# Performance work log

Hardware: AMD Instinct MI355X
Metric: run time of the kernel (lower is better)

Reference implementation:

```python
import jax, jax.numpy as jnp
import numpy as np

# Plane axes from generate_planes(); projection uses their inverses (permutation matrices).
_PLANES = np.array([[[1, 0, 0], [0, 1, 0], [0, 0, 1]],
                    [[1, 0, 0], [0, 0, 1], [0, 1, 0]],
                    [[0, 0, 1], [1, 0, 0], [0, 1, 0]]], dtype=np.float32)
_INV_PLANES = np.linalg.inv(_PLANES)  # [3,3,3]


def _grid_sample_2d(feat, grid):
    """Bilinear grid_sample, padding_mode='zeros', align_corners=False.
    feat: [C,H,W], grid: [M,2] with (x,y) in normalized coords. Returns [C,M]."""
    C, H, W = feat.shape
    x = ((grid[:, 0] + 1.0) * W - 1.0) * 0.5  # [M] pixel coords
    y = ((grid[:, 1] + 1.0) * H - 1.0) * 0.5
    x0 = jnp.floor(x)
    y0 = jnp.floor(y)
    wx = x - x0  # weight of right/bottom neighbor
    wy = y - y0
    x0i = x0.astype(jnp.int32)
    y0i = y0.astype(jnp.int32)
    x1i = x0i + 1
    y1i = y0i + 1

    def corner(xi, yi):
        valid = (xi >= 0) & (xi < W) & (yi >= 0) & (yi < H)
        xc = jnp.clip(xi, 0, W - 1)
        yc = jnp.clip(yi, 0, H - 1)
        v = feat[:, yc, xc]  # [C, M] gather
        return v * valid.astype(feat.dtype)

    v00 = corner(x0i, y0i)
    v10 = corner(x1i, y0i)
    v01 = corner(x0i, y1i)
    v11 = corner(x1i, y1i)
    out = (v00 * (1.0 - wx) * (1.0 - wy)
           + v10 * wx * (1.0 - wy)
           + v01 * (1.0 - wx) * wy
           + v11 * wx * wy)
    return out  # [C, M]


def setup_inputs() -> dict:
    key = jax.random.key(0)
    k1, k2, k3 = jax.random.split(key, 3)
    N, P, C, H, W, M = 4, 3, 32, 256, 256, 500000
    planes = jax.random.normal(k1, (N, P, C, H, W), dtype=jnp.float32)
    sample_coordinates = jax.random.uniform(k2, (N, M, 3), dtype=jnp.float32,
                                            minval=-1.0, maxval=1.0)
    sample_directions = jax.random.normal(k3, (N, M, 3), dtype=jnp.float32)
    return {"planes": planes, "sample_coordinates": sample_coordinates,
            "sample_directions": sample_directions}


def reference(planes, sample_coordinates, sample_directions):
    # ImportanceRenderer.run_model: project -> grid_sample per plane -> mean over planes.
    N, n_planes, C, H, W = planes.shape
    M = sample_coordinates.shape[1]
    inv = jnp.asarray(_INV_PLANES, dtype=sample_coordinates.dtype)  # [P,3,3]
    # torch.bmm(coords, inv_planes): [N,P,M,3] @ [P,3,3] -> take first 2 dims
    proj = jnp.einsum('nmi,pij->npmj', sample_coordinates, inv)[..., :2]  # [N,P,M,2]
    feats = planes.reshape(N * n_planes, C, H, W)
    grids = proj.reshape(N * n_planes, M, 2)
    sampled = jax.vmap(_grid_sample_2d)(feats, grids)  # [N*P, C, M]
    sampled = sampled.reshape(N, n_planes, C, M).transpose(0, 1, 3, 2)  # [N,P,M,C]
    return sampled.mean(axis=1)  # [N, M, C]
```

## Files before the change

### kernel.cpp

```cpp
#include <hip/hip_runtime.h>
#include <hip/hip_fp16.h>


constexpr int Cc = 32, Hh = 256, Ww = 256, Pp = 3, Nn = 4;
constexpr int HWPIX = Hh * Ww;
constexpr int NCO   = 4096;
constexpr int CAP   = 256;

typedef float f32x4 __attribute__((ext_vector_type(4)));

__device__ inline unsigned spread3(unsigned x) {
    x &= 0x3FFu;
    x = (x | (x << 16)) & 0x030000FFu;
    x = (x | (x << 8))  & 0x0300F00Fu;
    x = (x | (x << 4))  & 0x030C30C3u;
    x = (x | (x << 2))  & 0x09249249u;
    return x;
}
__device__ inline unsigned coarse_key(float cx, float cy, float cz) {
    const int a = min(max((int)((cx + 1.0f) * 8.0f), 0), 15);
    const int b = min(max((int)((cy + 1.0f) * 8.0f), 0), 15);
    const int c = min(max((int)((cz + 1.0f) * 8.0f), 0), 15);
    return spread3((unsigned)a) | (spread3((unsigned)b) << 1) | (spread3((unsigned)c) << 2);
}

__global__ __launch_bounds__(256) void transpose_chw_hwc_h(
    const float* __restrict__ in, __half* __restrict__ out)
{
    __shared__ float lds[Cc * 257];
    const int slice = blockIdx.y;
    const int pix0  = blockIdx.x * 256;
    const int t     = threadIdx.x;

    const float* src = in + (size_t)slice * Cc * HWPIX + pix0 + t;
    #pragma unroll
    for (int c = 0; c < Cc; ++c)
        lds[c * 257 + t] = src[(size_t)c * HWPIX];
    __syncthreads();

    uint4* dst = reinterpret_cast<uint4*>(
        out + (size_t)slice * HWPIX * Cc + (size_t)pix0 * Cc);
    #pragma unroll
    for (int k = 0; k < 4; ++k) {
        const int idx = k * 256 + t;
        const int pix = idx >> 2;
        const int c0  = (idx & 3) * 8;
        unsigned r[4];
        #pragma unroll
        for (int j = 0; j < 4; ++j) {
            const __half h0 = __float2half(lds[(c0 + 2 * j + 0) * 257 + pix]);
            const __half h1 = __float2half(lds[(c0 + 2 * j + 1) * 257 + pix]);
            r[j] = (unsigned)__half_as_ushort(h0)
                 | ((unsigned)__half_as_ushort(h1) << 16);
        }
        dst[idx] = make_uint4(r[0], r[1], r[2], r[3]);
    }
}

__global__ __launch_bounds__(256) void zero_u32(unsigned* __restrict__ p, int n)
{
    const int i = blockIdx.x * 256 + threadIdx.x;
    if (i < n) p[i] = 0u;
}

__global__ __launch_bounds__(256) void bin_scatter(
    const float* __restrict__ coords, unsigned* __restrict__ count,
    unsigned* __restrict__ tailcnt, unsigned* __restrict__ bin,
    unsigned* __restrict__ tail, int M)
{
    const int m = blockIdx.x * 256 + threadIdx.x;
    const int n = blockIdx.y;
    if (m >= M) return;
    const float* cp = coords + ((size_t)n * M + m) * 3;
    const unsigned k = coarse_key(cp[0], cp[1], cp[2]);
    const unsigned r = atomicAdd(&count[n * NCO + k], 1u);
    if (r < CAP) {
        bin[(((size_t)n * NCO + k) << 8) + r] = (unsigned)m;
    } else {
        const unsigned t = atomicAdd(&tailcnt[n], 1u);
        tail[(size_t)n * M + t] = (unsigned)m;
    }
}

__global__ __launch_bounds__(1024) void cell_scan_base(
    const unsigned* __restrict__ count, unsigned* __restrict__ base)
{
    __shared__ unsigned lds[1024];
    const unsigned* h = count + (size_t)blockIdx.x * NCO;
    unsigned* o = base + (size_t)blockIdx.x * NCO;
    const int t = threadIdx.x;
    unsigned v[4];
    unsigned s = 0;
    #pragma unroll
    for (int i = 0; i < 4; ++i) { v[i] = min(h[t * 4 + i], (unsigned)CAP); s += v[i]; }
    lds[t] = s;
    __syncthreads();
    for (int d = 1; d < 1024; d <<= 1) {
        const unsigned add = (t >= d) ? lds[t - d] : 0u;
        __syncthreads();
        lds[t] += add;
        __syncthreads();
    }
    unsigned b = (t > 0) ? lds[t - 1] : 0u;
    #pragma unroll
    for (int i = 0; i < 4; ++i) { const unsigned tmp = v[i]; o[t * 4 + i] = b; b += tmp; }
}

__global__ __launch_bounds__(256) void compact_cells(
    const unsigned* __restrict__ count, const unsigned* __restrict__ base,
    const unsigned* __restrict__ bin, unsigned* __restrict__ dense, int M)
{
    const int n = blockIdx.y, cell = blockIdx.x, t = threadIdx.x;
    const unsigned c = min(count[n * NCO + cell], (unsigned)CAP);
    if ((unsigned)t < c)
        dense[(size_t)n * M + base[n * NCO + cell] + t] =
            bin[(((size_t)n * NCO + cell) << 8) + t];
}

__global__ __launch_bounds__(256) void tail_copy(
    const unsigned* __restrict__ tailcnt, const unsigned* __restrict__ tail,
    unsigned* __restrict__ dense, int M)
{
    const int n = blockIdx.x;
    const unsigned tc = tailcnt[n];
    for (unsigned t = threadIdx.x; t < tc; t += 256)
        dense[(size_t)n * M + (M - tc) + t] = tail[(size_t)n * M + t];
}

__global__ __launch_bounds__(256) void triplane_gather4h(
    const __half* __restrict__ tp, const unsigned* __restrict__ idx,
    const float* __restrict__ coords, float* __restrict__ out,
    int M, int gx, int nwg)
{
    int bid = blockIdx.x;
    {
        const int q = nwg >> 3, r = nwg & 7;
        const int xcd = bid & 7, i = bid >> 3;
        bid = (xcd < r ? xcd * (q + 1) : r * (q + 1) + (xcd - r) * q) + i;
    }
    const int n  = bid / gx;
    const int bx = bid - n * gx;
    const int gid  = bx * 256 + threadIdx.x;
    const int s    = gid >> 2;
    const int quad = gid & 3;
    if (s >= M) return;

    const int m = (int)idx[(size_t)n * M + s];
    const float* cp = coords + ((size_t)n * M + m) * 3;
    const float cx = cp[0], cy = cp[1], cz = cp[2];

    const uint4* addr[12];
    __half2 wh[12];

    #pragma unroll
    for (int p = 0; p < 3; ++p) {
        const float gxc = (p == 2) ? cz : cx;
        const float gyc = (p == 0) ? cy : ((p == 1) ? cz : cx);
        const float x = ((gxc + 1.0f) * 256.0f - 1.0f) * 0.5f;
        const float y = ((gyc + 1.0f) * 256.0f - 1.0f) * 0.5f;
        const float x0f = floorf(x), y0f = floorf(y);
        const float wx = x - x0f, wy = y - y0f;
        const int x0 = (int)x0f, y0 = (int)y0f;
        const int x1 = x0 + 1,   y1 = y0 + 1;
        const bool vx0 = (unsigned)x0 < 256u;
        const bool vx1 = (unsigned)x1 < 256u;
        const bool vy0 = (unsigned)y0 < 256u;
        const bool vy1 = (unsigned)y1 < 256u;
        const int cx0 = min(max(x0, 0), 255), cx1 = min(max(x1, 0), 255);
        const int cy0 = min(max(y0, 0), 255), cy1 = min(max(y1, 0), 255);

        const float w00 = ((vx0 && vy0) ? 1.f : 0.f) * (1.f - wx) * (1.f - wy);
        const float w10 = ((vx1 && vy0) ? 1.f : 0.f) * wx * (1.f - wy);
        const float w01 = ((vx0 && vy1) ? 1.f : 0.f) * (1.f - wx) * wy;
        const float w11 = ((vx1 && vy1) ? 1.f : 0.f) * wx * wy;
        wh[p * 4 + 0] = __float2half2_rn(w00);
        wh[p * 4 + 1] = __float2half2_rn(w10);
        wh[p * 4 + 2] = __float2half2_rn(w01);
        wh[p * 4 + 3] = __float2half2_rn(w11);

        const uint4* base = reinterpret_cast<const uint4*>(
            tp + (size_t)(n * 3 + p) * HWPIX * Cc);
        addr[p * 4 + 0] = base + (size_t)((cy0 << 8) + cx0) * 4 + quad;
        addr[p * 4 + 1] = base + (size_t)((cy0 << 8) + cx1) * 4 + quad;
        addr[p * 4 + 2] = base + (size_t)((cy1 << 8) + cx0) * 4 + quad;
        addr[p * 4 + 3] = base + (size_t)((cy1 << 8) + cx1) * 4 + quad;
    }

    uint4 rv[12];
    #pragma unroll
    for (int j = 0; j < 12; ++j) rv[j] = *addr[j];

    float accx[8];
    #pragma unroll
    for (int i = 0; i < 8; ++i) accx[i] = 0.f;

    #pragma unroll
    for (int p = 0; p < 3; ++p) {
        __half2 a0 = __float2half2_rn(0.f), a1 = a0, a2 = a0, a3 = a0;
        #pragma unroll
        for (int c = 0; c < 4; ++c) {
            const uint4 v = rv[p * 4 + c];
            const __half2 w = wh[p * 4 + c];
            a0 = __hfma2(*reinterpret_cast<const __half2*>(&v.x), w, a0);
            a1 = __hfma2(*reinterpret_cast<const __half2*>(&v.y), w, a1);
            a2 = __hfma2(*reinterpret_cast<const __half2*>(&v.z), w, a2);
            a3 = __hfma2(*reinterpret_cast<const __half2*>(&v.w), w, a3);
        }
        const float2 f0 = __half22float2(a0);
        const float2 f1 = __half22float2(a1);
        const float2 f2 = __half22float2(a2);
        const float2 f3 = __half22float2(a3);
        accx[0] += f0.x; accx[1] += f0.y;
        accx[2] += f1.x; accx[3] += f1.y;
        accx[4] += f2.x; accx[5] += f2.y;
        accx[6] += f3.x; accx[7] += f3.y;
    }

    constexpr float third = 1.0f / 3.0f;
    f32x4 o0, o1;
    o0.x = accx[0] * third; o0.y = accx[1] * third;
    o0.z = accx[2] * third; o0.w = accx[3] * third;
    o1.x = accx[4] * third; o1.y = accx[5] * third;
    o1.z = accx[6] * third; o1.w = accx[7] * third;

    f32x4* op = reinterpret_cast<f32x4*>(out + ((size_t)n * M + m) * Cc);
    __builtin_nontemporal_store(o0, op + quad * 2 + 0);
    __builtin_nontemporal_store(o1, op + quad * 2 + 1);
}

__global__ __launch_bounds__(256) void triplane_gather_hwc8h(
    const __half* __restrict__ tp, const float* __restrict__ coords,
    float* __restrict__ out, int M)
{
    const int gid   = blockIdx.x * 256 + threadIdx.x;
    const int m     = gid >> 3;
    const int chunk = gid & 7;
    const int n     = blockIdx.y;
    if (m >= M) return;

    const float* cp = coords + ((size_t)n * M + m) * 3;
    const float cx = cp[0], cy = cp[1], cz = cp[2];

    const uint2* addr[12];
    float w[12];

    #pragma unroll
    for (int p = 0; p < 3; ++p) {
        const float gxc = (p == 2) ? cz : cx;
        const float gyc = (p == 0) ? cy : ((p == 1) ? cz : cx);
        const float x = ((gxc + 1.0f) * 256.0f - 1.0f) * 0.5f;
        const float y = ((gyc + 1.0f) * 256.0f - 1.0f) * 0.5f;
        const float x0f = floorf(x), y0f = floorf(y);
        const float wx = x - x0f, wy = y - y0f;
        const int x0 = (int)x0f, y0 = (int)y0f;
        const int x1 = x0 + 1,   y1 = y0 + 1;
        const bool vx0 = (unsigned)x0 < 256u;
        const bool vx1 = (unsigned)x1 < 256u;
        const bool vy0 = (unsigned)y0 < 256u;
        const bool vy1 = (unsigned)y1 < 256u;
        const int cx0 = min(max(x0, 0), 255), cx1 = min(max(x1, 0), 255);
        const int cy0 = min(max(y0, 0), 255), cy1 = min(max(y1, 0), 255);

        w[p * 4 + 0] = ((vx0 && vy0) ? 1.f : 0.f) * (1.f - wx) * (1.f - wy);
        w[p * 4 + 1] = ((vx1 && vy0) ? 1.f : 0.f) * wx * (1.f - wy);
        w[p * 4 + 2] = ((vx0 && vy1) ? 1.f : 0.f) * (1.f - wx) * wy;
        w[p * 4 + 3] = ((vx1 && vy1) ? 1.f : 0.f) * wx * wy;

        const uint2* base = reinterpret_cast<const uint2*>(
            tp + (size_t)(n * 3 + p) * HWPIX * Cc);
        addr[p * 4 + 0] = base + (size_t)((cy0 << 8) + cx0) * 8 + chunk;
        addr[p * 4 + 1] = base + (size_t)((cy0 << 8) + cx1) * 8 + chunk;
        addr[p * 4 + 2] = base + (size_t)((cy1 << 8) + cx0) * 8 + chunk;
        addr[p * 4 + 3] = base + (size_t)((cy1 << 8) + cx1) * 8 + chunk;
    }

    uint2 rv[12];
    #pragma unroll
    for (int j = 0; j < 12; ++j) rv[j] = *addr[j];

    float4 acc = make_float4(0.f, 0.f, 0.f, 0.f);
    #pragma unroll
    for (int j = 0; j < 12; ++j) {
        const __half2 h0 = *reinterpret_cast<const __half2*>(&rv[j].x);
        const __half2 h1 = *reinterpret_cast<const __half2*>(&rv[j].y);
        const float2 f0 = __half22float2(h0);
        const float2 f1 = __half22float2(h1);
        acc.x += w[j] * f0.x;
        acc.y += w[j] * f0.y;
        acc.z += w[j] * f1.x;
        acc.w += w[j] * f1.y;
    }

    constexpr float third = 1.0f / 3.0f;
    acc.x *= third; acc.y *= third; acc.z *= third; acc.w *= third;

    float4* op = reinterpret_cast<float4*>(out + ((size_t)n * M + m) * Cc);
    op[chunk] = acc;
}

__global__ __launch_bounds__(256) void triplane_gather_chw(
    const float* __restrict__ planes, const float* __restrict__ coords,
    float* __restrict__ out, int M)
{
    const int m = blockIdx.x * 256 + threadIdx.x;
    const int n = blockIdx.y;
    if (m >= M) return;

    const float* cp = coords + ((size_t)n * M + m) * 3;
    const float cx = cp[0], cy = cp[1], cz = cp[2];

    int   off[3][4];
    float w[3][4];
    #pragma unroll
    for (int p = 0; p < 3; ++p) {
        const float gxc = (p == 2) ? cz : cx;
        const float gyc = (p == 0) ? cy : ((p == 1) ? cz : cx);
        const float x = ((gxc + 1.0f) * 256.0f - 1.0f) * 0.5f;
        const float y = ((gyc + 1.0f) * 256.0f - 1.0f) * 0.5f;
        const float x0f = floorf(x), y0f = floorf(y);
        const float wx = x - x0f, wy = y - y0f;
        const int x0 = (int)x0f, y0 = (int)y0f;
        const int x1 = x0 + 1,   y1 = y0 + 1;
        const bool vx0 = (unsigned)x0 < 256u, vx1 = (unsigned)x1 < 256u;
        const bool vy0 = (unsigned)y0 < 256u, vy1 = (unsigned)y1 < 256u;
        const int cx0 = min(max(x0, 0), 255), cx1 = min(max(x1, 0), 255);
        const int cy0 = min(max(y0, 0), 255), cy1 = min(max(y1, 0), 255);
        off[p][0] = (cy0 << 8) + cx0;  w[p][0] = ((vx0 && vy0) ? 1.f : 0.f) * (1.f - wx) * (1.f - wy);
        off[p][1] = (cy0 << 8) + cx1;  w[p][1] = ((vx1 && vy0) ? 1.f : 0.f) * wx * (1.f - wy);
        off[p][2] = (cy1 << 8) + cx0;  w[p][2] = ((vx0 && vy1) ? 1.f : 0.f) * (1.f - wx) * wy;
        off[p][3] = (cy1 << 8) + cx1;  w[p][3] = ((vx1 && vy1) ? 1.f : 0.f) * wx * wy;
    }

    float* op = out + ((size_t)n * M + m) * Cc;
    constexpr float third = 1.0f / 3.0f;
    for (int c = 0; c < Cc; ++c) {
        float a = 0.f;
        #pragma unroll
        for (int p = 0; p < 3; ++p) {
            const float* b = planes + ((size_t)(n * 3 + p) * Cc + c) * HWPIX;
            a += w[p][0] * b[off[p][0]] + w[p][1] * b[off[p][1]]
               + w[p][2] * b[off[p][2]] + w[p][3] * b[off[p][3]];
        }
        op[c] = a * third;
    }
}

extern "C" void kernel_launch(void* const* d_in, const int* in_sizes, int n_in,
                              void* d_out, int out_size, void* d_ws, size_t ws_size,
                              hipStream_t stream)
{
    const float* planes = (const float*)d_in[0];
    const float* coords = (const float*)d_in[1];
    float* out = (float*)d_out;

    const int M = in_sizes[1] / (Nn * 3);

    auto align256 = [](size_t x) { return (x + 255) & ~(size_t)255; };
    const size_t tph_bytes   = align256((size_t)Nn * Pp * HWPIX * Cc * sizeof(__half));
    const size_t bin_bytes   = align256((size_t)Nn * NCO * CAP * sizeof(unsigned));
    const size_t dense_bytes = align256((size_t)Nn * M * sizeof(unsigned));
    const size_t tail_bytes  = align256((size_t)Nn * M * sizeof(unsigned));
    const size_t cnt_bytes   = align256((size_t)Nn * NCO * sizeof(unsigned));
    const size_t base_bytes  = align256((size_t)Nn * NCO * sizeof(unsigned));
    const size_t tc_bytes    = align256((size_t)Nn * sizeof(unsigned));

    const size_t need = tph_bytes + bin_bytes + dense_bytes + tail_bytes +
                        cnt_bytes + base_bytes + tc_bytes;

    if (ws_size >= need) {
        char* p = (char*)d_ws;
        __half*   tp      = (__half*)p;   p += tph_bytes;
        unsigned* bin     = (unsigned*)p; p += bin_bytes;
        unsigned* dense   = (unsigned*)p; p += dense_bytes;
        unsigned* tail    = (unsigned*)p; p += tail_bytes;
        unsigned* count   = (unsigned*)p; p += cnt_bytes;
        unsigned* base    = (unsigned*)p; p += base_bytes;
        unsigned* tailcnt = (unsigned*)p;

        transpose_chw_hwc_h<<<dim3(HWPIX / 256, Nn * Pp), 256, 0, stream>>>(planes, tp);
        zero_u32<<<(Nn * NCO + 255) / 256, 256, 0, stream>>>(count, Nn * NCO);
        zero_u32<<<1, 256, 0, stream>>>(tailcnt, Nn);
        bin_scatter<<<dim3((M + 255) / 256, Nn), 256, 0, stream>>>(
            coords, count, tailcnt, bin, tail, M);
        cell_scan_base<<<Nn, 1024, 0, stream>>>(count, base);
        compact_cells<<<dim3(NCO, Nn), 256, 0, stream>>>(count, base, bin, dense, M);
        tail_copy<<<Nn, 256, 0, stream>>>(tailcnt, tail, dense, M);

        const int gx  = (M * 4 + 255) / 256;
        const int nwg = Nn * gx;
        triplane_gather4h<<<nwg, 256, 0, stream>>>(tp, dense, coords, out, M, gx, nwg);
    } else if (ws_size >= tph_bytes) {
        __half* tp = (__half*)d_ws;
        transpose_chw_hwc_h<<<dim3(HWPIX / 256, Nn * Pp), 256, 0, stream>>>(planes, tp);
        const int gx = (M * 8 + 255) / 256;
        triplane_gather_hwc8h<<<dim3(gx, Nn), 256, 0, stream>>>(tp, coords, out, M);
    } else {
        const int gx = (M + 255) / 256;
        triplane_gather_chw<<<dim3(gx, Nn), 256, 0, stream>>>(planes, coords, out, M);
    }
}
```

Before: 285.0 us.

## Fuse transpose with binning and gather directly from per-cell bins

The plane transpose and the coordinate binning now run as one launch, with separate block ranges doing each job. The prefix-scan, compaction and tail-copy kernels are removed. The gather kernel instead assigns one workgroup per spatial cell, or per tail chunk, and reads point indices straight from the bins. The count and tail-count buffers, which sit next to each other, are cleared with a single zero kernel. This cuts several launches and the dense-index round trip through memory, at the cost of uneven work per workgroup, because cells hold very different numbers of points and workgroups loop in steps of 64.

```diff
diff --git a/kernel.cpp b/kernel.cpp
--- a/kernel.cpp
+++ b/kernel.cpp
@@ -6,6 +6,8 @@
 constexpr int HWPIX = Hh * Ww;
 constexpr int NCO   = 4096;
 constexpr int CAP   = 256;
+constexpr int TAILB = 64;
+constexpr int TRB   = Nn * Pp * (HWPIX / 256);
 
 typedef float f32x4 __attribute__((ext_vector_type(4)));
 
@@ -24,128 +26,70 @@
     return spread3((unsigned)a) | (spread3((unsigned)b) << 1) | (spread3((unsigned)c) << 2);
 }
 
-__global__ __launch_bounds__(256) void transpose_chw_hwc_h(
-    const float* __restrict__ in, __half* __restrict__ out)
-{
-    __shared__ float lds[Cc * 257];
-    const int slice = blockIdx.y;
-    const int pix0  = blockIdx.x * 256;
-    const int t     = threadIdx.x;
-
-    const float* src = in + (size_t)slice * Cc * HWPIX + pix0 + t;
-    #pragma unroll
-    for (int c = 0; c < Cc; ++c)
-        lds[c * 257 + t] = src[(size_t)c * HWPIX];
-    __syncthreads();
-
-    uint4* dst = reinterpret_cast<uint4*>(
-        out + (size_t)slice * HWPIX * Cc + (size_t)pix0 * Cc);
-    #pragma unroll
-    for (int k = 0; k < 4; ++k) {
-        const int idx = k * 256 + t;
-        const int pix = idx >> 2;
-        const int c0  = (idx & 3) * 8;
-        unsigned r[4];
-        #pragma unroll
-        for (int j = 0; j < 4; ++j) {
-            const __half h0 = __float2half(lds[(c0 + 2 * j + 0) * 257 + pix]);
-            const __half h1 = __float2half(lds[(c0 + 2 * j + 1) * 257 + pix]);
-            r[j] = (unsigned)__half_as_ushort(h0)
-                 | ((unsigned)__half_as_ushort(h1) << 16);
-        }
-        dst[idx] = make_uint4(r[0], r[1], r[2], r[3]);
-    }
-}
-
 __global__ __launch_bounds__(256) void zero_u32(unsigned* __restrict__ p, int n)
 {
     const int i = blockIdx.x * 256 + threadIdx.x;
     if (i < n) p[i] = 0u;
 }
 
-__global__ __launch_bounds__(256) void bin_scatter(
-    const float* __restrict__ coords, unsigned* __restrict__ count,
+__global__ __launch_bounds__(256) void fused_tb(
+    const float* __restrict__ planes, const float* __restrict__ coords,
+    __half* __restrict__ tp, unsigned* __restrict__ count,
     unsigned* __restrict__ tailcnt, unsigned* __restrict__ bin,
-    unsigned* __restrict__ tail, int M)
-{
-    const int m = blockIdx.x * 256 + threadIdx.x;
-    const int n = blockIdx.y;
-    if (m >= M) return;
-    const float* cp = coords + ((size_t)n * M + m) * 3;
-    const unsigned k = coarse_key(cp[0], cp[1], cp[2]);
-    const unsigned r = atomicAdd(&count[n * NCO + k], 1u);
-    if (r < CAP) {
-        bin[(((size_t)n * NCO + k) << 8) + r] = (unsigned)m;
+    unsigned* __restrict__ tail, int M, int binBlocksPerN)
+{
+    __shared__ float lds[Cc * 257];
+    const int t = threadIdx.x;
+
+    if (blockIdx.x < TRB) {
+        const int slice = blockIdx.x >> 8;
+        const int pix0  = (blockIdx.x & 255) * 256;
+
+        const float* src = planes + (size_t)slice * Cc * HWPIX + pix0 + t;
+        #pragma unroll
+        for (int c = 0; c < Cc; ++c)
+            lds[c * 257 + t] = src[(size_t)c * HWPIX];
+        __syncthreads();
+
+        uint4* dst = reinterpret_cast<uint4*>(
+            tp + (size_t)slice * HWPIX * Cc + (size_t)pix0 * Cc);
+        #pragma unroll
+        for (int k = 0; k < 4; ++k) {
+            const int idx = k * 256 + t;
+            const int pix = idx >> 2;
+            const int c0  = (idx & 3) * 8;
+            unsigned r[4];
+            #pragma unroll
+            for (int j = 0; j < 4; ++j) {
+                const __half h0 = __float2half(lds[(c0 + 2 * j + 0) * 257 + pix]);
+                const __half h1 = __float2half(lds[(c0 + 2 * j + 1) * 257 + pix]);
+                r[j] = (unsigned)__half_as_ushort(h0)
+                     | ((unsigned)__half_as_ushort(h1) << 16);
+            }
+            dst[idx] = make_uint4(r[0], r[1], r[2], r[3]);
+        }
     } else {
-        const unsigned t = atomicAdd(&tailcnt[n], 1u);
-        tail[(size_t)n * M + t] = (unsigned)m;
-    }
-}
-
-__global__ __launch_bounds__(1024) void cell_scan_base(
-    const unsigned* __restrict__ count, unsigned* __restrict__ base)
-{
-    __shared__ unsigned lds[1024];
-    const unsigned* h = count + (size_t)blockIdx.x * NCO;
-    unsigned* o = base + (size_t)blockIdx.x * NCO;
-    const int t = threadIdx.x;
-    unsigned v[4];
-    unsigned s = 0;
-    #pragma unroll
-    for (int i = 0; i < 4; ++i) { v[i] = min(h[t * 4 + i], (unsigned)CAP); s += v[i]; }
-    lds[t] = s;
-    __syncthreads();
-    for (int d = 1; d < 1024; d <<= 1) {
-        const unsigned add = (t >= d) ? lds[t - d] : 0u;
-        __syncthreads();
-        lds[t] += add;
-        __syncthreads();
-    }
-    unsigned b = (t > 0) ? lds[t - 1] : 0u;
-    #pragma unroll
-    for (int i = 0; i < 4; ++i) { const unsigned tmp = v[i]; o[t * 4 + i] = b; b += tmp; }
-}
-
-__global__ __launch_bounds__(256) void compact_cells(
-    const unsigned* __restrict__ count, const unsigned* __restrict__ base,
-    const unsigned* __restrict__ bin, unsigned* __restrict__ dense, int M)
-{
-    const int n = blockIdx.y, cell = blockIdx.x, t = threadIdx.x;
-    const unsigned c = min(count[n * NCO + cell], (unsigned)CAP);
-    if ((unsigned)t < c)
-        dense[(size_t)n * M + base[n * NCO + cell] + t] =
-            bin[(((size_t)n * NCO + cell) << 8) + t];
-}
-
-__global__ __launch_bounds__(256) void tail_copy(
-    const unsigned* __restrict__ tailcnt, const unsigned* __restrict__ tail,
-    unsigned* __restrict__ dense, int M)
-{
-    const int n = blockIdx.x;
-    const unsigned tc = tailcnt[n];
-    for (unsigned t = threadIdx.x; t < tc; t += 256)
-        dense[(size_t)n * M + (M - tc) + t] = tail[(size_t)n * M + t];
-}
-
-__global__ __launch_bounds__(256) void triplane_gather4h(
-    const __half* __restrict__ tp, const unsigned* __restrict__ idx,
-    const float* __restrict__ coords, float* __restrict__ out,
-    int M, int gx, int nwg)
-{
-    int bid = blockIdx.x;
-    {
-        const int q = nwg >> 3, r = nwg & 7;
-        const int xcd = bid & 7, i = bid >> 3;
-        bid = (xcd < r ? xcd * (q + 1) : r * (q + 1) + (xcd - r) * q) + i;
-    }
-    const int n  = bid / gx;
-    const int bx = bid - n * gx;
-    const int gid  = bx * 256 + threadIdx.x;
-    const int s    = gid >> 2;
-    const int quad = gid & 3;
-    if (s >= M) return;
-
-    const int m = (int)idx[(size_t)n * M + s];
+        const int j = blockIdx.x - TRB;
+        const int n = j / binBlocksPerN;
+        const int m = (j - n * binBlocksPerN) * 256 + t;
+        if (m < M) {
+            const float* cp = coords + ((size_t)n * M + m) * 3;
+            const unsigned k = coarse_key(cp[0], cp[1], cp[2]);
+            const unsigned r = atomicAdd(&count[n * NCO + k], 1u);
+            if (r < CAP) {
+                bin[(((size_t)n * NCO + k) << 8) + r] = (unsigned)m;
+            } else {
+                const unsigned tt = atomicAdd(&tailcnt[n], 1u);
+                tail[(size_t)n * M + tt] = (unsigned)m;
+            }
+        }
+    }
+}
+
+__device__ __forceinline__ void gather_one(
+    const __half* __restrict__ tp, const float* __restrict__ coords,
+    float* __restrict__ out, int n, int m, int quad, int M)
+{
     const float* cp = coords + ((size_t)n * M + m) * 3;
     const float cx = cp[0], cy = cp[1], cz = cp[2];
 
@@ -226,6 +170,76 @@
     f32x4* op = reinterpret_cast<f32x4*>(out + ((size_t)n * M + m) * Cc);
     __builtin_nontemporal_store(o0, op + quad * 2 + 0);
     __builtin_nontemporal_store(o1, op + quad * 2 + 1);
+}
+
+__global__ __launch_bounds__(256) void gather_cells(
+    const __half* __restrict__ tp, const unsigned* __restrict__ count,
+    const unsigned* __restrict__ tailcnt, const unsigned* __restrict__ bin,
+    const unsigned* __restrict__ tail, const float* __restrict__ coords,
+    float* __restrict__ out, int M, int nwg)
+{
+    int bid = blockIdx.x;
+    {
+        const int q = nwg >> 3, r = nwg & 7;
+        const int xcd = bid & 7, i = bid >> 3;
+        bid = (xcd < r ? xcd * (q + 1) : r * (q + 1) + (xcd - r) * q) + i;
+    }
+    constexpr int PER_N = NCO + TAILB;
+    const int n  = bid / PER_N;
+    const int cb = bid - n * PER_N;
+    const int t  = threadIdx.x;
+    const int ls = t >> 2;
+    const int quad = t & 3;
+
+    if (cb < NCO) {
+        unsigned c = count[n * NCO + cb];
+        c = (c > (unsigned)CAP) ? (unsigned)CAP : c;
+        const unsigned* bp = bin + (((size_t)n * NCO + cb) << 8);
+        for (unsigned base = 0; base < c; base += 64) {
+            const unsigned j = base + ls;
+            if (j < c)
+                gather_one(tp, coords, out, n, (int)bp[j], quad, M);
+        }
+    } else {
+        unsigned tc = tailcnt[n];
+        if (tc > (unsigned)M) tc = (unsigned)M;
+        for (unsigned s = (unsigned)(cb - NCO) * 64 + ls; s < tc;
+             s += (unsigned)TAILB * 64)
+            gather_one(tp, coords, out, n, (int)tail[(size_t)n * M + s], quad, M);
+    }
+}
+
+__global__ __launch_bounds__(256) void transpose_chw_hwc_h(
+    const float* __restrict__ in, __half* __restrict__ out)
+{
+    __shared__ float lds[Cc * 257];
+    const int slice = blockIdx.y;
+    const int pix0  = blockIdx.x * 256;
+    const int t     = threadIdx.x;
+
+    const float* src = in + (size_t)slice * Cc * HWPIX + pix0 + t;
+    #pragma unroll
+    for (int c = 0; c < Cc; ++c)
+        lds[c * 257 + t] = src[(size_t)c * HWPIX];
+    __syncthreads();
+
+    uint4* dst = reinterpret_cast<uint4*>(
+        out + (size_t)slice * HWPIX * Cc + (size_t)pix0 * Cc);
+    #pragma unroll
+    for (int k = 0; k < 4; ++k) {
+        const int idx = k * 256 + t;
+        const int pix = idx >> 2;
+        const int c0  = (idx & 3) * 8;
+        unsigned r[4];
+        #pragma unroll
+        for (int j = 0; j < 4; ++j) {
+            const __half h0 = __float2half(lds[(c0 + 2 * j + 0) * 257 + pix]);
+            const __half h1 = __float2half(lds[(c0 + 2 * j + 1) * 257 + pix]);
+            r[j] = (unsigned)__half_as_ushort(h0)
+                 | ((unsigned)__half_as_ushort(h1) << 16);
+        }
+        dst[idx] = make_uint4(r[0], r[1], r[2], r[3]);
+    }
 }
 
 __global__ __launch_bounds__(256) void triplane_gather_hwc8h(
@@ -356,39 +370,31 @@
     const int M = in_sizes[1] / (Nn * 3);
 
     auto align256 = [](size_t x) { return (x + 255) & ~(size_t)255; };
-    const size_t tph_bytes   = align256((size_t)Nn * Pp * HWPIX * Cc * sizeof(__half));
-    const size_t bin_bytes   = align256((size_t)Nn * NCO * CAP * sizeof(unsigned));
-    const size_t dense_bytes = align256((size_t)Nn * M * sizeof(unsigned));
-    const size_t tail_bytes  = align256((size_t)Nn * M * sizeof(unsigned));
-    const size_t cnt_bytes   = align256((size_t)Nn * NCO * sizeof(unsigned));
-    const size_t base_bytes  = align256((size_t)Nn * NCO * sizeof(unsigned));
-    const size_t tc_bytes    = align256((size_t)Nn * sizeof(unsigned));
-
-    const size_t need = tph_bytes + bin_bytes + dense_bytes + tail_bytes +
-                        cnt_bytes + base_bytes + tc_bytes;
-
-    if (ws_size >= need) {
+    const size_t tph_bytes  = align256((size_t)Nn * Pp * HWPIX * Cc * sizeof(__half));
+    const size_t bin_bytes  = align256((size_t)Nn * NCO * CAP * sizeof(unsigned));
+    const size_t tail_bytes = align256((size_t)Nn * M * sizeof(unsigned));
+    const size_t cnt_bytes  = align256((size_t)Nn * NCO * sizeof(unsigned));
+    const size_t tc_bytes   = align256((size_t)Nn * sizeof(unsigned));
+
+    if (ws_size >= tph_bytes + bin_bytes + tail_bytes + cnt_bytes + tc_bytes) {
         char* p = (char*)d_ws;
         __half*   tp      = (__half*)p;   p += tph_bytes;
         unsigned* bin     = (unsigned*)p; p += bin_bytes;
-        unsigned* dense   = (unsigned*)p; p += dense_bytes;
         unsigned* tail    = (unsigned*)p; p += tail_bytes;
         unsigned* count   = (unsigned*)p; p += cnt_bytes;
-        unsigned* base    = (unsigned*)p; p += base_bytes;
         unsigned* tailcnt = (unsigned*)p;
 
-        transpose_chw_hwc_h<<<dim3(HWPIX / 256, Nn * Pp), 256, 0, stream>>>(planes, tp);
-        zero_u32<<<(Nn * NCO + 255) / 256, 256, 0, stream>>>(count, Nn * NCO);
-        zero_u32<<<1, 256, 0, stream>>>(tailcnt, Nn);
-        bin_scatter<<<dim3((M + 255) / 256, Nn), 256, 0, stream>>>(
-            coords, count, tailcnt, bin, tail, M);
-        cell_scan_base<<<Nn, 1024, 0, stream>>>(count, base);
-        compact_cells<<<dim3(NCO, Nn), 256, 0, stream>>>(count, base, bin, dense, M);
-        tail_copy<<<Nn, 256, 0, stream>>>(tailcnt, tail, dense, M);
-
-        const int gx  = (M * 4 + 255) / 256;
-        const int nwg = Nn * gx;
-        triplane_gather4h<<<nwg, 256, 0, stream>>>(tp, dense, coords, out, M, gx, nwg);
+        const int nz = Nn * NCO + Nn;
+        zero_u32<<<(nz + 255) / 256, 256, 0, stream>>>(count, nz);
+
+        const int binBlocksPerN = (M + 255) / 256;
+        const int k1 = TRB + Nn * binBlocksPerN;
+        fused_tb<<<k1, 256, 0, stream>>>(planes, coords, tp, count, tailcnt,
+                                         bin, tail, M, binBlocksPerN);
+
+        const int nwg = Nn * (NCO + TAILB);
+        gather_cells<<<nwg, 256, 0, stream>>>(tp, count, tailcnt, bin, tail,
+                                              coords, out, M, nwg);
     } else if (ws_size >= tph_bytes) {
         __half* tp = (__half*)d_ws;
         transpose_chw_hwc_h<<<dim3(HWPIX / 256, Nn * Pp), 256, 0, stream>>>(planes, tp);
```

Result: no change. 286.1 us (+0.4%).
